# Kernel optimization log

Measured on AMD Instinct MI355X. Metric: run time of the kernel, lower is better.

The kernel has to match this reference:

```python
import jax, jax.numpy as jnp
import numpy as np

# TT config (matches init_kwargs)
NUM_TABLES = 4
P = (100, 100, 100)          # tt_p_shapes, prod = num_embeddings = 1e6
Q = (4, 4, 4)                # tt_q_shapes, prod = embedding_dim = 64
R = (1, 32, 32, 1)           # tt_ranks with boundary ranks
BAGS_PER_TABLE = 8192
POOL = 16                    # indices per bag


def setup_inputs() -> dict:
    key = jax.random.key(0)
    k1, k2, k3, k4 = jax.random.split(key, 4)
    nnz = NUM_TABLES * BAGS_PER_TABLE * POOL      # 524288
    B = NUM_TABLES * BAGS_PER_TABLE               # 32768 bags total
    indices = jax.random.randint(k1, (nnz,), 0, P[0] * P[1] * P[2], dtype=jnp.int64)
    offsets = (jnp.arange(B + 1, dtype=jnp.int64) * POOL)
    scale = 0.05  # small init, akin to approx-normal weight_dist
    tt_core_0 = jax.random.normal(k2, (NUM_TABLES, P[0], R[0] * Q[0] * R[1]), dtype=jnp.float32) * scale
    tt_core_1 = jax.random.normal(k3, (NUM_TABLES, P[1], R[1] * Q[1] * R[2]), dtype=jnp.float32) * scale
    tt_core_2 = jax.random.normal(k4, (NUM_TABLES, P[2], R[2] * Q[2] * R[3]), dtype=jnp.float32) * scale
    return {"indices": indices, "offsets": offsets,
            "tt_core_0": tt_core_0, "tt_core_1": tt_core_1, "tt_core_2": tt_core_2}


def reference(indices, offsets, tt_core_0, tt_core_1, tt_core_2):
    nnz = indices.shape[0]
    B = offsets.shape[0] - 1
    bags_per_table = B // NUM_TABLES

    # bag id for each nonzero (embedding-bag semantics), then table id per nonzero
    rowidx = jnp.searchsorted(offsets, jnp.arange(nnz, dtype=offsets.dtype), side='right') - 1
    tableidx = rowidx // bags_per_table

    # decompose flat row index into TT indices (C-order over p-shapes,
    # matching tt_matrix_to_full row layout)
    i0 = indices // (P[1] * P[2])
    i1 = (indices // P[2]) % P[1]
    i2 = indices % P[2]

    # gather per-lookup core slices
    c0 = tt_core_0[tableidx, i0].reshape(nnz, Q[0], R[1])          # r0 == 1
    c1 = tt_core_1[tableidx, i1].reshape(nnz, R[1], Q[1], R[2])
    c2 = tt_core_2[tableidx, i2].reshape(nnz, R[2], Q[2])          # r3 == 1

    # on-the-fly TT contraction to reconstruct embedding rows [nnz, D]
    t = jnp.einsum('nar,nrbs->nabs', c0, c1)                       # [nnz, q0, q1, r2]
    rows = jnp.einsum('nabs,nsc->nabc', t, c2).reshape(nnz, Q[0] * Q[1] * Q[2])

    # sum-pool per bag
    out = jax.ops.segment_sum(rows, rowidx, num_segments=B)        # [B, D]
    return out
```

## Files before the change

kernel.cpp:

```cpp
#include <hip/hip_runtime.h>
#include <stdint.h>

#define NT 4
#define PP 100
#define TT_BYTES (4ull * 100 * 100 * 1024)


__device__ __forceinline__ uint32_t f2bf(float f) {
    union { float f; uint32_t u; } v; v.f = f;
    uint32_t u = v.u;
    return (u + 0x7fffu + ((u >> 16) & 1u)) >> 16;
}

__device__ __forceinline__ float dot2bf(uint32_t a, uint32_t b, float c) {
    float d;
    asm("v_dot2_f32_bf16 %0, %1, %2, %3" : "=v"(d) : "v"(a), "v"(b), "v"(c));
    return d;
}

__global__ __launch_bounds__(256)
void c2pack_kernel(const float* __restrict__ c2g, uint32_t* __restrict__ c2p) {
    int t = blockIdx.x * 256 + threadIdx.x;
    if (t >= NT * PP * 64) return;
    int c = t & 3, sg = (t >> 2) & 15, rest = t >> 6;
    int i2 = rest % PP, tab = rest / PP;
    const float* src = c2g + (size_t)(tab * PP + i2) * 128;
    float e = src[(2 * sg) * 4 + c];
    float o = src[(2 * sg + 1) * 4 + c];
    c2p[t] = f2bf(e) | (f2bf(o) << 16);
}

__global__ __launch_bounds__(128, 3)
void tt_phase1(const float* __restrict__ c0g, const float* __restrict__ c1g,
               unsigned short* __restrict__ tT) {
    __shared__ float c1s[32 * 128];
    __shared__ float c0t[16 * 132];

    int blk = blockIdx.x;
    int tab   = blk / 700;
    int rem   = blk % 700;
    int i1    = rem / 7;
    int chunk = rem % 7;
    int i0_base = chunk * 16;
    int tid = threadIdx.x;

    const float4* c1p = (const float4*)(c1g + (size_t)(tab * PP + i1) * 4096);
    float4* c1v = (float4*)c1s;
    #pragma unroll
    for (int it = 0; it < 8; ++it) c1v[tid + 128 * it] = c1p[tid + 128 * it];

    #pragma unroll
    for (int it = 0; it < 16; ++it) {
        int f = tid + 128 * it;
        int i0l = f >> 7;
        int x   = f & 127;
        int a = x >> 5, r = x & 31;
        int i0 = i0_base + i0l; if (i0 > PP - 1) i0 = PP - 1;
        c0t[i0l * 132 + r * 4 + a] = c0g[(size_t)(tab * PP + i0) * 128 + x];
    }
    __syncthreads();

    int u  = tid >> 4;
    int sg = tid & 15;

    float acc[2][2][16];
    #pragma unroll
    for (int ii = 0; ii < 2; ++ii)
        #pragma unroll
        for (int e = 0; e < 2; ++e)
            #pragma unroll
            for (int q = 0; q < 16; ++q) acc[ii][e][q] = 0.f;

    #pragma unroll 4
    for (int r = 0; r < 32; ++r) {
        float4 av0 = *(const float4*)&c0t[(2 * u) * 132 + r * 4];
        float4 av1 = *(const float4*)&c0t[(2 * u + 1) * 132 + r * 4];
        const float* a0 = (const float*)&av0;
        const float* a1 = (const float*)&av1;
        #pragma unroll
        for (int b = 0; b < 4; ++b) {
            float2 bv = *(const float2*)&c1s[r * 128 + b * 32 + 2 * sg];
            #pragma unroll
            for (int a = 0; a < 4; ++a) {
                acc[0][0][a * 4 + b] += a0[a] * bv.x;
                acc[0][1][a * 4 + b] += a0[a] * bv.y;
                acc[1][0][a * 4 + b] += a1[a] * bv.x;
                acc[1][1][a * 4 + b] += a1[a] * bv.y;
            }
        }
    }

    #pragma unroll
    for (int ii = 0; ii < 2; ++ii) {
        int i0 = i0_base + 2 * u + ii;
        if (i0 >= PP) continue;
        size_t combo = (size_t)tab * 10000 + (size_t)i0 * 100 + (size_t)i1;
        char* base = (char*)tT + combo * 1024 + (size_t)sg * 64;
        #pragma unroll
        for (int k = 0; k < 4; ++k) {
            uint4 w;
            w.x = f2bf(acc[ii][0][4*k+0]) | (f2bf(acc[ii][1][4*k+0]) << 16);
            w.y = f2bf(acc[ii][0][4*k+1]) | (f2bf(acc[ii][1][4*k+1]) << 16);
            w.z = f2bf(acc[ii][0][4*k+2]) | (f2bf(acc[ii][1][4*k+2]) << 16);
            w.w = f2bf(acc[ii][0][4*k+3]) | (f2bf(acc[ii][1][4*k+3]) << 16);
            *(uint4*)(base + k * 16) = w;
        }
    }
}

__global__ __launch_bounds__(256, 3)
void tt_phase2(const int* __restrict__ indices, const int* __restrict__ offsets,
               const unsigned short* __restrict__ tT, const uint32_t* __restrict__ c2p,
               float* __restrict__ out, int bags_per_table, int B) {
    int lane = threadIdx.x & 63;
    int wv   = threadIdx.x >> 6;
    int bag  = blockIdx.x * 4 + wv;
    if (bag >= B) return;
    int sub = lane >> 4;
    int sg  = lane & 15;
    int tab = bag / bags_per_table;
    int start = offsets[bag];

    const uint4* c2q = (const uint4*)c2p;

    const uint4* tp[4];
    int ci[4];
    #pragma unroll
    for (int j = 0; j < 4; ++j) {
        uint32_t idx = (uint32_t)indices[start + j * 4 + sub];
        uint32_t i0 = idx / 10000u;
        uint32_t r1 = idx - i0 * 10000u;
        uint32_t i1 = r1 / 100u;
        uint32_t i2 = r1 - i1 * 100u;
        tp[j] = (const uint4*)((const char*)tT +
                 ((size_t)tab * 10000u + i0 * 100u + i1) * 1024 + (size_t)sg * 64);
        ci[j] = (tab * PP + (int)i2) * 16 + sg;
    }

    uint4 T[4][4];
    uint4 C[4];
    #pragma unroll
    for (int j = 0; j < 4; ++j) {
        T[j][0] = tp[j][0]; T[j][1] = tp[j][1];
        T[j][2] = tp[j][2]; T[j][3] = tp[j][3];
        C[j] = c2q[ci[j]];
    }

    float acc[64];
    #pragma unroll
    for (int d = 0; d < 64; ++d) acc[d] = 0.f;

    #pragma unroll
    for (int j = 0; j < 4; ++j) {
        uint32_t cd[4] = { C[j].x, C[j].y, C[j].z, C[j].w };
        #pragma unroll
        for (int k = 0; k < 4; ++k) {
            uint32_t td[4] = { T[j][k].x, T[j][k].y, T[j][k].z, T[j][k].w };
            #pragma unroll
            for (int m = 0; m < 4; ++m) {
                int d0 = (4 * k + m) * 4;
                acc[d0 + 0] = dot2bf(td[m], cd[0], acc[d0 + 0]);
                acc[d0 + 1] = dot2bf(td[m], cd[1], acc[d0 + 1]);
                acc[d0 + 2] = dot2bf(td[m], cd[2], acc[d0 + 2]);
                acc[d0 + 3] = dot2bf(td[m], cd[3], acc[d0 + 3]);
            }
        }
    }

    #pragma unroll
    for (int m = 32; m >= 1; m >>= 1) {
        bool up = (lane & m) != 0;
        #pragma unroll
        for (int j = 0; j < m; ++j) {
            float lo = acc[j], hi = acc[j + m];
            float send = up ? lo : hi;
            float recv = __shfl_xor(send, m, 64);
            acc[j] = (up ? hi : lo) + recv;
        }
    }
    out[(size_t)bag * 64 + lane] = acc[0];
}

extern "C" void kernel_launch(void* const* d_in, const int* in_sizes, int n_in,
                              void* d_out, int out_size, void* d_ws, size_t ws_size,
                              hipStream_t stream) {
    const int*   indices = (const int*)d_in[0];
    const int*   offsets = (const int*)d_in[1];
    const float* c0      = (const float*)d_in[2];
    const float* c1      = (const float*)d_in[3];
    const float* c2      = (const float*)d_in[4];
    float* out = (float*)d_out;

    int B = in_sizes[1] - 1;
    int bags_per_table = B / NT;

    unsigned short* tT  = (unsigned short*)d_ws;
    uint32_t*       c2p = (uint32_t*)((char*)d_ws + TT_BYTES);

    c2pack_kernel<<<dim3((NT * PP * 64 + 255) / 256), dim3(256), 0, stream>>>(c2, c2p);
    tt_phase1<<<dim3(NT * PP * 7), dim3(128), 0, stream>>>(c0, c1, tT);
    tt_phase2<<<dim3((B + 3) / 4), dim3(256), 0, stream>>>(indices, offsets, tT, c2p, out,
                                                           bags_per_table, B);
}
```

Before: 155.1 us.

## Fuse c2 packing into phase1, pin tables to XCDs, vectorize index loads

Folds the c2 bf16 packing kernel into the first 200 blocks of phase1, which removes one kernel launch. Changes the LDS padding stride from 132 to 136 and drops the min-blocks launch bounds on both kernels. Remaps phase2 blocks so that each table's bags land on a fixed pair of XCDs, keeping that table's tT slice hot in the local L2. Also loads the four indices per lane with a single int4 read instead of four scalar reads. The XCD mapping assumes round-robin block placement across eight XCDs, and the int4 load assumes 16-byte-aligned bag starts, which holds for pool size 16.

```diff
diff --git a/kernel.cpp b/kernel.cpp
--- a/kernel.cpp
+++ b/kernel.cpp
@@ -18,31 +18,31 @@
     return d;
 }
 
-__global__ __launch_bounds__(256)
-void c2pack_kernel(const float* __restrict__ c2g, uint32_t* __restrict__ c2p) {
-    int t = blockIdx.x * 256 + threadIdx.x;
-    if (t >= NT * PP * 64) return;
-    int c = t & 3, sg = (t >> 2) & 15, rest = t >> 6;
-    int i2 = rest % PP, tab = rest / PP;
-    const float* src = c2g + (size_t)(tab * PP + i2) * 128;
-    float e = src[(2 * sg) * 4 + c];
-    float o = src[(2 * sg + 1) * 4 + c];
-    c2p[t] = f2bf(e) | (f2bf(o) << 16);
-}
-
-__global__ __launch_bounds__(128, 3)
+__global__ __launch_bounds__(128)
 void tt_phase1(const float* __restrict__ c0g, const float* __restrict__ c1g,
-               unsigned short* __restrict__ tT) {
+               const float* __restrict__ c2g, unsigned short* __restrict__ tT,
+               uint32_t* __restrict__ c2p) {
     __shared__ float c1s[32 * 128];
-    __shared__ float c0t[16 * 132];
+    __shared__ float c0t[16 * 136];
 
     int blk = blockIdx.x;
+    int tid = threadIdx.x;
+
+    if (blk < 200) {
+        int t = blk * 128 + tid;
+        int c = t & 3, sg2 = (t >> 2) & 15, rest = t >> 6;
+        int i2 = rest % PP, tb = rest / PP;
+        const float* src = c2g + (size_t)(tb * PP + i2) * 128;
+        float e = src[(2 * sg2) * 4 + c];
+        float o = src[(2 * sg2 + 1) * 4 + c];
+        c2p[t] = f2bf(e) | (f2bf(o) << 16);
+    }
+
     int tab   = blk / 700;
     int rem   = blk % 700;
     int i1    = rem / 7;
     int chunk = rem % 7;
     int i0_base = chunk * 16;
-    int tid = threadIdx.x;
 
     const float4* c1p = (const float4*)(c1g + (size_t)(tab * PP + i1) * 4096);
     float4* c1v = (float4*)c1s;
@@ -56,7 +56,7 @@
         int x   = f & 127;
         int a = x >> 5, r = x & 31;
         int i0 = i0_base + i0l; if (i0 > PP - 1) i0 = PP - 1;
-        c0t[i0l * 132 + r * 4 + a] = c0g[(size_t)(tab * PP + i0) * 128 + x];
+        c0t[i0l * 136 + r * 4 + a] = c0g[(size_t)(tab * PP + i0) * 128 + x];
     }
     __syncthreads();
 
@@ -73,8 +73,8 @@
 
     #pragma unroll 4
     for (int r = 0; r < 32; ++r) {
-        float4 av0 = *(const float4*)&c0t[(2 * u) * 132 + r * 4];
-        float4 av1 = *(const float4*)&c0t[(2 * u + 1) * 132 + r * 4];
+        float4 av0 = *(const float4*)&c0t[(2 * u) * 136 + r * 4];
+        float4 av1 = *(const float4*)&c0t[(2 * u + 1) * 136 + r * 4];
         const float* a0 = (const float*)&av0;
         const float* a1 = (const float*)&av1;
         #pragma unroll
@@ -108,26 +108,40 @@
     }
 }
 
-__global__ __launch_bounds__(256, 3)
+__global__ __launch_bounds__(256)
 void tt_phase2(const int* __restrict__ indices, const int* __restrict__ offsets,
                const unsigned short* __restrict__ tT, const uint32_t* __restrict__ c2p,
                float* __restrict__ out, int bags_per_table, int B) {
     int lane = threadIdx.x & 63;
     int wv   = threadIdx.x >> 6;
-    int bag  = blockIdx.x * 4 + wv;
+    int blk  = blockIdx.x;
+
+    int tab, bag;
+    if (((gridDim.x & 7) == 0) && ((B & 31) == 0)) {
+        int xcd = blk & 7;
+        tab = xcd >> 1;
+        int within = ((blk >> 3) << 1) + (xcd & 1);
+        bag = tab * bags_per_table + within * 4 + wv;
+    } else {
+        bag = blk * 4 + wv;
+        tab = bag / bags_per_table;
+    }
     if (bag >= B) return;
+
     int sub = lane >> 4;
     int sg  = lane & 15;
-    int tab = bag / bags_per_table;
     int start = offsets[bag];
 
     const uint4* c2q = (const uint4*)c2p;
+
+    int4 iv = *(const int4*)&indices[start + 4 * sub];
+    int ivs[4] = { iv.x, iv.y, iv.z, iv.w };
 
     const uint4* tp[4];
     int ci[4];
     #pragma unroll
     for (int j = 0; j < 4; ++j) {
-        uint32_t idx = (uint32_t)indices[start + j * 4 + sub];
+        uint32_t idx = (uint32_t)ivs[j];
         uint32_t i0 = idx / 10000u;
         uint32_t r1 = idx - i0 * 10000u;
         uint32_t i1 = r1 / 100u;
@@ -197,8 +211,7 @@
     unsigned short* tT  = (unsigned short*)d_ws;
     uint32_t*       c2p = (uint32_t*)((char*)d_ws + TT_BYTES);
 
-    c2pack_kernel<<<dim3((NT * PP * 64 + 255) / 256), dim3(256), 0, stream>>>(c2, c2p);
-    tt_phase1<<<dim3(NT * PP * 7), dim3(128), 0, stream>>>(c0, c1, tT);
+    tt_phase1<<<dim3(NT * PP * 7), dim3(128), 0, stream>>>(c0, c1, c2, tT, c2p);
     tt_phase2<<<dim3((B + 3) / 4), dim3(256), 0, stream>>>(indices, offsets, tT, c2p, out,
                                                            bags_per_table, B);
 }
```

Measured after the change: 162.9 us. +5.0%, slower.
